# Kernel optimization log

Hardware: AMD Instinct MI355X
Metric: run time of the kernel (lower is better)

Reference implementation:

```python
import jax, jax.numpy as jnp
import numpy as np

HIDDEN = 256
N_HEADS = 8
HEAD_DIM = HIDDEN // N_HEADS
SCALE = HEAD_DIM ** -0.5
LN_EPS = 1e-5


def entmax15(z):
    """Entmax-1.5 along the last axis (Peters et al. 2019 exact algorithm)."""
    z = z / 2.0
    z = z - jnp.max(z, axis=-1, keepdims=True)
    zs = jnp.flip(jnp.sort(z, axis=-1), axis=-1)          # descending
    K = z.shape[-1]
    k = jnp.arange(1, K + 1, dtype=z.dtype)
    mean = jnp.cumsum(zs, axis=-1) / k
    mean_sq = jnp.cumsum(zs * zs, axis=-1) / k
    ss = k * (mean_sq - mean * mean)
    delta = (1.0 - ss) / k
    tau = mean - jnp.sqrt(jnp.maximum(delta, 1e-12))
    support = (tau <= zs).astype(jnp.int32)
    k_star = jnp.sum(support, axis=-1, keepdims=True)      # support size >=1
    tau_star = jnp.take_along_axis(tau, k_star - 1, axis=-1)
    p = jnp.square(jnp.maximum(z - tau_star, 0.0))
    return p


def _attend(q, kv, W_q, W_k, W_v, log_temp):
    B, K, H = kv.shape
    qh = (q @ W_q.T).reshape(B, N_HEADS, HEAD_DIM)                 # (B,n,d)
    kh = (kv @ W_k.T).reshape(B, K, N_HEADS, HEAD_DIM)             # (B,K,n,d)
    vh = (kv @ W_v.T).reshape(B, K, N_HEADS, HEAD_DIM)
    scores = jnp.einsum('bnd,bknd->bnk', qh, kh) * (SCALE * jnp.exp(log_temp))
    attn = entmax15(scores)                                        # (B,n,K) sparse
    ctx = jnp.einsum('bnk,bknd->bnd', attn, vh).reshape(B, H)
    return ctx


def layernorm(x, gamma, beta):
    mu = jnp.mean(x, axis=-1, keepdims=True)
    var = jnp.mean(jnp.square(x - mu), axis=-1, keepdims=True)
    return (x - mu) * jax.lax.rsqrt(var + LN_EPS) * gamma + beta


def setup_inputs() -> dict:
    key = jax.random.key(0)
    ks = jax.random.split(key, 12)
    B, K, H = 32, 8192, HIDDEN
    s = 0.02
    return {
        'z_gene': jax.random.normal(ks[0], (B, H), jnp.float32),
        'z_cpg_seq': jax.random.normal(ks[1], (B, K, H), jnp.float32),
        'z_mirna_seq': jax.random.normal(ks[2], (B, K, H), jnp.float32),
        'W_q': jax.random.normal(ks[3], (H, H), jnp.float32) * s,
        'W_k_cpg': jax.random.normal(ks[4], (H, H), jnp.float32) * s,
        'W_v_cpg': jax.random.normal(ks[5], (H, H), jnp.float32) * s,
        'W_k_mirna': jax.random.normal(ks[6], (H, H), jnp.float32) * s,
        'W_v_mirna': jax.random.normal(ks[7], (H, H), jnp.float32) * s,
        'W_out': jax.random.normal(ks[8], (H, 2 * H), jnp.float32) * s,
        'b_out': jnp.zeros((H,), jnp.float32),
        'ln_gamma': jnp.ones((H,), jnp.float32),
        'ln_beta': jnp.zeros((H,), jnp.float32),
        'modality_logits': jnp.zeros((2,), jnp.float32),
        'log_temp': jnp.zeros((), jnp.float32),
    }


def reference(z_gene, z_cpg_seq, z_mirna_seq, W_q, W_k_cpg, W_v_cpg,
              W_k_mirna, W_v_mirna, W_out, b_out, ln_gamma, ln_beta,
              modality_logits, log_temp):
    ctx_cpg = _attend(z_gene, z_cpg_seq, W_q, W_k_cpg, W_v_cpg, log_temp)
    ctx_mirna = _attend(z_gene, z_mirna_seq, W_q, W_k_mirna, W_v_mirna, log_temp)
    w = jax.nn.softmax(modality_logits)
    combined = jnp.concatenate([w[0] * ctx_cpg, w[1] * ctx_mirna], axis=-1)
    fused = layernorm(combined @ W_out.T + b_out + z_gene, ln_gamma, ln_beta)
    return fused
```

## Files before the change

### kernel.cpp

```cpp
#include <hip/hip_runtime.h>
#include <cstdint>
#include <cstddef>

#define HIDDEN 256
#define NHEADS 8
#define HDIM 32
#define KLEN 8192
#define BATCH 32
#define NCHUNK 16
#define CHUNK (KLEN / NCHUNK)
#define NCHUNK_S 32
#define CROWS (KLEN / NCHUNK_S)
#define LN_EPS 1e-5f

#define OFF_QT   ((size_t)0)
#define SZ_QT    ((size_t)2*BATCH*NHEADS*HIDDEN)
#define OFF_SC   (OFF_QT + SZ_QT)
#define SZ_SC    ((size_t)2*BATCH*KLEN*NHEADS)
#define OFF_UP   (OFF_SC + SZ_SC)
#define SZ_UP    ((size_t)2*BATCH*NCHUNK*NHEADS*HIDDEN)
#define OFF_COMB (OFF_UP + SZ_UP)
#define SZ_COMB  ((size_t)BATCH*2*HIDDEN)

__global__ void k_prep(const float* __restrict__ zg, const float* __restrict__ Wq,
                       const float* __restrict__ Wk0, const float* __restrict__ Wk1,
                       const float* __restrict__ log_temp, float* __restrict__ qt) {
    int b = blockIdx.x, t = threadIdx.x;
    __shared__ float z[HIDDEN];
    __shared__ float qh[HIDDEN];
    z[t] = zg[(size_t)b*HIDDEN + t];
    __syncthreads();
    const float4* wr4 = (const float4*)(Wq + (size_t)t*HIDDEN);
    const float4* z4 = (const float4*)z;
    float acc = 0.f;
    #pragma unroll 8
    for (int i = 0; i < HIDDEN/4; ++i) {
        float4 w = wr4[i], zz = z4[i];
        acc += w.x*zz.x + w.y*zz.y + w.z*zz.z + w.w*zz.w;
    }
    qh[t] = acc;
    __syncthreads();
    float alpha = 0.5f * rsqrtf((float)HDIM) * __expf(log_temp[0]);
    for (int m = 0; m < 2; ++m) {
        const float* Wk = m ? Wk1 : Wk0;
        for (int n = 0; n < NHEADS; ++n) {
            float a = 0.f;
            #pragma unroll 8
            for (int d = 0; d < HDIM; ++d) {
                a += qh[n*HDIM + d] * Wk[(size_t)(n*HDIM + d)*HIDDEN + t];
            }
            qt[(((size_t)m*BATCH + b)*NHEADS + n)*HIDDEN + t] = a * alpha;
        }
    }
}

__global__ void __launch_bounds__(256, 4) k_scores(const float* __restrict__ kv0,
                                                   const float* __restrict__ kv1,
                                                   const float* __restrict__ qt,
                                                   float* __restrict__ sc) {
    int bid = blockIdx.x;
    int chunk = bid % NCHUNK_S;
    int m = (bid / NCHUNK_S) & 1;
    int b = bid / (2*NCHUNK_S);
    int t = threadIdx.x;
    int wave = t >> 6;
    int g    = (t >> 3) & 7;
    int seg  = t & 7;
    __shared__ float lq[NHEADS*260];
    const float* qtg = qt + ((size_t)m*BATCH + b)*NHEADS*HIDDEN;
    #pragma unroll
    for (int i = 0; i < 8; ++i) {
        int j = t + i*256;
        lq[(j >> 8)*260 + (j & 255)] = qtg[j];
    }
    __syncthreads();
    const float* kv = (m ? kv1 : kv0) + (size_t)b*KLEN*HIDDEN;
    const float4* kv4 = (const float4*)kv;
    float* out = sc + ((size_t)m*BATCH + b)*KLEN*NHEADS;
    int b0 = seg & 1, b1 = (seg >> 1) & 1, b2 = (seg >> 2) & 1;

    #pragma unroll
    for (int pass = 0; pass < 2; ++pass) {
        size_t r = (size_t)chunk*CROWS + wave*64 + pass*32 + g*4;
        float acc[4][8];
        #pragma unroll
        for (int j = 0; j < 4; ++j)
            #pragma unroll
            for (int n = 0; n < 8; ++n) acc[j][n] = 0.f;
        #pragma unroll 2
        for (int i = 0; i < 8; ++i) {
            int c = i*8 + seg;
            float4 k0 = kv4[(r+0)*64 + c];
            float4 k1 = kv4[(r+1)*64 + c];
            float4 k2 = kv4[(r+2)*64 + c];
            float4 k3 = kv4[(r+3)*64 + c];
            #pragma unroll
            for (int n = 0; n < 8; ++n) {
                float4 q = ((const float4*)(lq + n*260))[c];
                acc[0][n] += k0.x*q.x + k0.y*q.y + k0.z*q.z + k0.w*q.w;
                acc[1][n] += k1.x*q.x + k1.y*q.y + k1.z*q.z + k1.w*q.w;
                acc[2][n] += k2.x*q.x + k2.y*q.y + k2.z*q.z + k2.w*q.w;
                acc[3][n] += k3.x*q.x + k3.y*q.y + k3.z*q.z + k3.w*q.w;
            }
        }
        #pragma unroll
        for (int j = 0; j < 4; ++j) {
            float w[4];
            #pragma unroll
            for (int u = 0; u < 4; ++u) {
                float kkeep = b0 ? acc[j][2*u+1] : acc[j][2*u];
                float ksend = b0 ? acc[j][2*u]   : acc[j][2*u+1];
                w[u] = kkeep + __shfl_xor(ksend, 1);
            }
            float x[2];
            #pragma unroll
            for (int u = 0; u < 2; ++u) {
                float kkeep = b1 ? w[2*u+1] : w[2*u];
                float ksend = b1 ? w[2*u]   : w[2*u+1];
                x[u] = kkeep + __shfl_xor(ksend, 2);
            }
            float kkeep = b2 ? x[1] : x[0];
            float ksend = b2 ? x[0] : x[1];
            float y = kkeep + __shfl_xor(ksend, 4);
            out[(r+j)*8 + seg] = y;
        }
    }
}

__global__ void __launch_bounds__(256) k_entmax(float* __restrict__ sc) {
    int bid = blockIdx.x;
    int n = bid & 7, b = (bid >> 3) & 31, m = bid >> 8;
    int t = threadIdx.x;
    __shared__ float zs[KLEN];
    __shared__ float red[4];
    float* src = sc + ((size_t)m*BATCH + b)*KLEN*NHEADS + n;
    float mx = -1e30f;
    #pragma unroll
    for (int i = 0; i < KLEN/256; ++i) {
        float v = src[(size_t)(t + i*256)*NHEADS];
        zs[t + i*256] = v;
        mx = fmaxf(mx, v);
    }
    for (int off = 32; off; off >>= 1) mx = fmaxf(mx, __shfl_xor(mx, off));
    if ((t & 63) == 0) red[t >> 6] = mx;
    __syncthreads();
    mx = fmaxf(fmaxf(red[0], red[1]), fmaxf(red[2], red[3]));
    __syncthreads();
    const float4* z4 = (const float4*)zs;
    float lo = mx - 1.0f, hi = mx;
    for (int it = 0; it < 26; ++it) {
        float tm = 0.5f*(lo + hi);
        float s = 0.f;
        #pragma unroll
        for (int i = 0; i < 8; ++i) {
            float4 zz = z4[t + i*256];
            float d;
            d = fmaxf(zz.x - tm, 0.f); s = fmaf(d, d, s);
            d = fmaxf(zz.y - tm, 0.f); s = fmaf(d, d, s);
            d = fmaxf(zz.z - tm, 0.f); s = fmaf(d, d, s);
            d = fmaxf(zz.w - tm, 0.f); s = fmaf(d, d, s);
        }
        for (int off = 32; off; off >>= 1) s += __shfl_xor(s, off);
        if ((t & 63) == 0) red[t >> 6] = s;
        __syncthreads();
        s = red[0] + red[1] + red[2] + red[3];
        __syncthreads();
        if (s >= 1.0f) lo = tm; else hi = tm;
    }
    float tfin = 0.5f*(lo + hi);
    #pragma unroll
    for (int i = 0; i < KLEN/256; ++i) {
        float d = fmaxf(zs[t + i*256] - tfin, 0.f);
        src[(size_t)(t + i*256)*NHEADS] = d*d;
    }
}

__global__ void __launch_bounds__(256, 4) k_ctxsum(const float* __restrict__ kv0,
                                                   const float* __restrict__ kv1,
                                                   const float* __restrict__ sc,
                                                   float* __restrict__ upart) {
    int bid = (int)gridDim.x - 1 - (int)blockIdx.x;
    int chunk = bid % NCHUNK;
    int m = (bid / NCHUNK) & 1;
    int b = bid / (2*NCHUNK);
    int t = threadIdx.x;
    int wave = t >> 6, lane = t & 63;
    const float* kv = (m ? kv1 : kv0) + (size_t)b*KLEN*HIDDEN;
    const float4* kv4 = (const float4*)kv;
    const float4* prow4 = (const float4*)(sc + ((size_t)m*BATCH + b)*KLEN*NHEADS);
    float acc[8][4];
    #pragma unroll
    for (int nn = 0; nn < 8; ++nn)
        #pragma unroll
        for (int c = 0; c < 4; ++c) acc[nn][c] = 0.f;

    for (int kb = wave*4; kb < CHUNK; kb += 16) {
        size_t k = (size_t)chunk*CHUNK + kb;
        float4 kva = kv4[(k+0)*64 + lane];
        float4 kvb = kv4[(k+1)*64 + lane];
        float4 kvc = kv4[(k+2)*64 + lane];
        float4 kvd = kv4[(k+3)*64 + lane];
        float4 pa0 = prow4[(k+0)*2], pa1 = prow4[(k+0)*2 + 1];
        float4 pb0 = prow4[(k+1)*2], pb1 = prow4[(k+1)*2 + 1];
        float4 pc0 = prow4[(k+2)*2], pc1 = prow4[(k+2)*2 + 1];
        float4 pd0 = prow4[(k+3)*2], pd1 = prow4[(k+3)*2 + 1];
        #define ACC4(P0, P1, KV) \
            acc[0][0] = fmaf(P0.x, KV.x, acc[0][0]); acc[0][1] = fmaf(P0.x, KV.y, acc[0][1]); \
            acc[0][2] = fmaf(P0.x, KV.z, acc[0][2]); acc[0][3] = fmaf(P0.x, KV.w, acc[0][3]); \
            acc[1][0] = fmaf(P0.y, KV.x, acc[1][0]); acc[1][1] = fmaf(P0.y, KV.y, acc[1][1]); \
            acc[1][2] = fmaf(P0.y, KV.z, acc[1][2]); acc[1][3] = fmaf(P0.y, KV.w, acc[1][3]); \
            acc[2][0] = fmaf(P0.z, KV.x, acc[2][0]); acc[2][1] = fmaf(P0.z, KV.y, acc[2][1]); \
            acc[2][2] = fmaf(P0.z, KV.z, acc[2][2]); acc[2][3] = fmaf(P0.z, KV.w, acc[2][3]); \
            acc[3][0] = fmaf(P0.w, KV.x, acc[3][0]); acc[3][1] = fmaf(P0.w, KV.y, acc[3][1]); \
            acc[3][2] = fmaf(P0.w, KV.z, acc[3][2]); acc[3][3] = fmaf(P0.w, KV.w, acc[3][3]); \
            acc[4][0] = fmaf(P1.x, KV.x, acc[4][0]); acc[4][1] = fmaf(P1.x, KV.y, acc[4][1]); \
            acc[4][2] = fmaf(P1.x, KV.z, acc[4][2]); acc[4][3] = fmaf(P1.x, KV.w, acc[4][3]); \
            acc[5][0] = fmaf(P1.y, KV.x, acc[5][0]); acc[5][1] = fmaf(P1.y, KV.y, acc[5][1]); \
            acc[5][2] = fmaf(P1.y, KV.z, acc[5][2]); acc[5][3] = fmaf(P1.y, KV.w, acc[5][3]); \
            acc[6][0] = fmaf(P1.z, KV.x, acc[6][0]); acc[6][1] = fmaf(P1.z, KV.y, acc[6][1]); \
            acc[6][2] = fmaf(P1.z, KV.z, acc[6][2]); acc[6][3] = fmaf(P1.z, KV.w, acc[6][3]); \
            acc[7][0] = fmaf(P1.w, KV.x, acc[7][0]); acc[7][1] = fmaf(P1.w, KV.y, acc[7][1]); \
            acc[7][2] = fmaf(P1.w, KV.z, acc[7][2]); acc[7][3] = fmaf(P1.w, KV.w, acc[7][3]);
        ACC4(pa0, pa1, kva)
        ACC4(pb0, pb1, kvb)
        ACC4(pc0, pc1, kvc)
        ACC4(pd0, pd1, kvd)
        #undef ACC4
    }
    __shared__ float redls[4*NHEADS*HIDDEN];
    float4* red4 = (float4*)redls;
    #pragma unroll
    for (int nn = 0; nn < 8; ++nn) {
        float4 v; v.x = acc[nn][0]; v.y = acc[nn][1]; v.z = acc[nn][2]; v.w = acc[nn][3];
        red4[((size_t)wave*8 + nn)*64 + lane] = v;
    }
    __syncthreads();
    float* up = upart + (((size_t)m*BATCH + b)*NCHUNK + chunk)*NHEADS*HIDDEN;
    int n = t >> 5, hq = (t & 31)*2;
    #pragma unroll
    for (int j = 0; j < 2; ++j) {
        float4 s = red4[((size_t)0*8 + n)*64 + hq + j];
        #pragma unroll
        for (int w = 1; w < 4; ++w) {
            float4 v = red4[((size_t)w*8 + n)*64 + hq + j];
            s.x += v.x; s.y += v.y; s.z += v.z; s.w += v.w;
        }
        ((float4*)(up + (size_t)n*HIDDEN))[hq + j] = s;
    }
}

__global__ void k_ctx(const float* __restrict__ upart, const float* __restrict__ Wv0,
                      const float* __restrict__ Wv1, const float* __restrict__ mlogits,
                      float* __restrict__ comb) {
    int b = blockIdx.x, t = threadIdx.x;
    __shared__ float ul[NHEADS*260];
    float l0 = mlogits[0], l1 = mlogits[1];
    float mxl = fmaxf(l0, l1);
    float e0 = __expf(l0 - mxl), e1 = __expf(l1 - mxl);
    float w0 = e0/(e0 + e1), w1 = e1/(e0 + e1);
    for (int m = 0; m < 2; ++m) {
        const float* Wv = m ? Wv1 : Wv0;
        float wm = m ? w1 : w0;
        __syncthreads();
        for (int n = 0; n < NHEADS; ++n) {
            float s = 0.f;
            const float* up = upart + ((size_t)m*BATCH + b)*NCHUNK*NHEADS*HIDDEN
                              + (size_t)n*HIDDEN + t;
            #pragma unroll
            for (int c = 0; c < NCHUNK; ++c) s += up[(size_t)c*NHEADS*HIDDEN];
            ul[n*260 + t] = s;
        }
        __syncthreads();
        int n = t >> 5;
        const float4* wr4 = (const float4*)(Wv + (size_t)t*HIDDEN);
        const float4* uu4 = (const float4*)(ul + n*260);
        float acc = 0.f;
        #pragma unroll 8
        for (int i = 0; i < HIDDEN/4; ++i) {
            float4 w = wr4[i], uu = uu4[i];
            acc += w.x*uu.x + w.y*uu.y + w.z*uu.z + w.w*uu.w;
        }
        comb[(size_t)b*(2*HIDDEN) + (size_t)m*HIDDEN + t] = acc * wm;
    }
}

__global__ void k_out(const float* __restrict__ comb, const float* __restrict__ Wout,
                      const float* __restrict__ bout, const float* __restrict__ zg,
                      const float* __restrict__ gamma, const float* __restrict__ beta,
                      float* __restrict__ out) {
    int b = blockIdx.x, t = threadIdx.x;
    __shared__ float cl[2*HIDDEN];
    __shared__ float red[4];
    cl[t] = comb[(size_t)b*512 + t];
    cl[t + 256] = comb[(size_t)b*512 + 256 + t];
    __syncthreads();
    float acc = bout[t] + zg[(size_t)b*HIDDEN + t];
    const float4* wr4 = (const float4*)(Wout + (size_t)t*512);
    const float4* cl4 = (const float4*)cl;
    #pragma unroll 8
    for (int i = 0; i < 512/4; ++i) {
        float4 w = wr4[i], c = cl4[i];
        acc += w.x*c.x + w.y*c.y + w.z*c.z + w.w*c.w;
    }
    float s = acc;
    for (int off = 32; off; off >>= 1) s += __shfl_xor(s, off);
    if ((t & 63) == 0) red[t >> 6] = s;
    __syncthreads();
    float mu = (red[0] + red[1] + red[2] + red[3]) * (1.0f/HIDDEN);
    __syncthreads();
    float dv = acc - mu;
    float vs = dv*dv;
    for (int off = 32; off; off >>= 1) vs += __shfl_xor(vs, off);
    if ((t & 63) == 0) red[t >> 6] = vs;
    __syncthreads();
    float var = (red[0] + red[1] + red[2] + red[3]) * (1.0f/HIDDEN);
    out[(size_t)b*HIDDEN + t] = dv * rsqrtf(var + LN_EPS) * gamma[t] + beta[t];
}

extern "C" void kernel_launch(void* const* d_in, const int* in_sizes, int n_in,
                              void* d_out, int out_size, void* d_ws, size_t ws_size,
                              hipStream_t stream) {
    const float* zg    = (const float*)d_in[0];
    const float* cpg   = (const float*)d_in[1];
    const float* mir   = (const float*)d_in[2];
    const float* Wq    = (const float*)d_in[3];
    const float* Wk0   = (const float*)d_in[4];
    const float* Wv0   = (const float*)d_in[5];
    const float* Wk1   = (const float*)d_in[6];
    const float* Wv1   = (const float*)d_in[7];
    const float* Wout  = (const float*)d_in[8];
    const float* bout  = (const float*)d_in[9];
    const float* gam   = (const float*)d_in[10];
    const float* bet   = (const float*)d_in[11];
    const float* mlog  = (const float*)d_in[12];
    const float* ltemp = (const float*)d_in[13];

    float* ws   = (float*)d_ws;
    float* qt   = ws + OFF_QT;
    float* sc   = ws + OFF_SC;
    float* up   = ws + OFF_UP;
    float* comb = ws + OFF_COMB;
    float* out  = (float*)d_out;

    hipLaunchKernelGGL(k_prep,   dim3(BATCH),             dim3(256), 0, stream,
                       zg, Wq, Wk0, Wk1, ltemp, qt);
    hipLaunchKernelGGL(k_scores, dim3(BATCH*2*NCHUNK_S),  dim3(256), 0, stream,
                       cpg, mir, qt, sc);
    hipLaunchKernelGGL(k_entmax, dim3(2*BATCH*NHEADS),    dim3(256), 0, stream,
                       sc);
    hipLaunchKernelGGL(k_ctxsum, dim3(BATCH*2*NCHUNK),    dim3(256), 0, stream,
                       cpg, mir, sc, up);
    hipLaunchKernelGGL(k_ctx,    dim3(BATCH),             dim3(256), 0, stream,
                       up, Wv0, Wv1, mlog, comb);
    hipLaunchKernelGGL(k_out,    dim3(BATCH),             dim3(256), 0, stream,
                       comb, Wout, bout, zg, gam, bet, out);
}
```

Baseline: 338.4 us.

## Compact entmax support rows and gather only nonzero rows in context sum

Adds a k_support kernel that builds, per (modality, batch), a compacted list of key rows where any head has nonzero entmax weight. k_ctxsum then reads only those rows instead of streaming the full 8192-row KV. The aim is to cut the second full read of the KV tensors, since entmax output is sparse. k_scores is also restructured: more chunks, a single pass per thread, and manual software pipelining of the loads. The cost is an extra launch, a serial scan in k_support, and scattered row reads whose speed depends on how sparse the weights are.

```diff
diff --git a/kernel.cpp b/kernel.cpp
--- a/kernel.cpp
+++ b/kernel.cpp
@@ -7,20 +7,23 @@
 #define HDIM 32
 #define KLEN 8192
 #define BATCH 32
-#define NCHUNK 16
-#define CHUNK (KLEN / NCHUNK)
-#define NCHUNK_S 32
+#define NCHUNK_S 64
 #define CROWS (KLEN / NCHUNK_S)
+#define NSPLIT 8
 #define LN_EPS 1e-5f
 
-#define OFF_QT   ((size_t)0)
-#define SZ_QT    ((size_t)2*BATCH*NHEADS*HIDDEN)
-#define OFF_SC   (OFF_QT + SZ_QT)
-#define SZ_SC    ((size_t)2*BATCH*KLEN*NHEADS)
-#define OFF_UP   (OFF_SC + SZ_SC)
-#define SZ_UP    ((size_t)2*BATCH*NCHUNK*NHEADS*HIDDEN)
-#define OFF_COMB (OFF_UP + SZ_UP)
-#define SZ_COMB  ((size_t)BATCH*2*HIDDEN)
+#define OFF_QT    ((size_t)0)
+#define SZ_QT     ((size_t)2*BATCH*NHEADS*HIDDEN)
+#define OFF_SC    (OFF_QT + SZ_QT)
+#define SZ_SC     ((size_t)2*BATCH*KLEN*NHEADS)
+#define OFF_UP    (OFF_SC + SZ_SC)
+#define SZ_UP     ((size_t)2*BATCH*NSPLIT*NHEADS*HIDDEN)
+#define OFF_COMB  (OFF_UP + SZ_UP)
+#define SZ_COMB   ((size_t)BATCH*2*HIDDEN)
+#define OFF_SLIST (OFF_COMB + SZ_COMB)
+#define SZ_SLIST  ((size_t)2*BATCH*KLEN)
+#define OFF_SCNT  (OFF_SLIST + SZ_SLIST)
+#define SZ_SCNT   ((size_t)2*BATCH)
 
 __global__ void k_prep(const float* __restrict__ zg, const float* __restrict__ Wq,
                        const float* __restrict__ Wk0, const float* __restrict__ Wk1,
@@ -63,9 +66,8 @@
     int m = (bid / NCHUNK_S) & 1;
     int b = bid / (2*NCHUNK_S);
     int t = threadIdx.x;
-    int wave = t >> 6;
-    int g    = (t >> 3) & 7;
-    int seg  = t & 7;
+    int gg  = t >> 3;
+    int seg = t & 7;
     __shared__ float lq[NHEADS*260];
     const float* qtg = qt + ((size_t)m*BATCH + b)*NHEADS*HIDDEN;
     #pragma unroll
@@ -79,51 +81,65 @@
     float* out = sc + ((size_t)m*BATCH + b)*KLEN*NHEADS;
     int b0 = seg & 1, b1 = (seg >> 1) & 1, b2 = (seg >> 2) & 1;
 
-    #pragma unroll
-    for (int pass = 0; pass < 2; ++pass) {
-        size_t r = (size_t)chunk*CROWS + wave*64 + pass*32 + g*4;
-        float acc[4][8];
-        #pragma unroll
-        for (int j = 0; j < 4; ++j)
-            #pragma unroll
-            for (int n = 0; n < 8; ++n) acc[j][n] = 0.f;
-        #pragma unroll 2
-        for (int i = 0; i < 8; ++i) {
-            int c = i*8 + seg;
-            float4 k0 = kv4[(r+0)*64 + c];
-            float4 k1 = kv4[(r+1)*64 + c];
-            float4 k2 = kv4[(r+2)*64 + c];
-            float4 k3 = kv4[(r+3)*64 + c];
-            #pragma unroll
-            for (int n = 0; n < 8; ++n) {
-                float4 q = ((const float4*)(lq + n*260))[c];
-                acc[0][n] += k0.x*q.x + k0.y*q.y + k0.z*q.z + k0.w*q.w;
-                acc[1][n] += k1.x*q.x + k1.y*q.y + k1.z*q.z + k1.w*q.w;
-                acc[2][n] += k2.x*q.x + k2.y*q.y + k2.z*q.z + k2.w*q.w;
-                acc[3][n] += k3.x*q.x + k3.y*q.y + k3.z*q.z + k3.w*q.w;
-            }
-        }
-        #pragma unroll
-        for (int j = 0; j < 4; ++j) {
-            float w[4];
-            #pragma unroll
-            for (int u = 0; u < 4; ++u) {
-                float kkeep = b0 ? acc[j][2*u+1] : acc[j][2*u];
-                float ksend = b0 ? acc[j][2*u]   : acc[j][2*u+1];
-                w[u] = kkeep + __shfl_xor(ksend, 1);
-            }
-            float x[2];
-            #pragma unroll
-            for (int u = 0; u < 2; ++u) {
-                float kkeep = b1 ? w[2*u+1] : w[2*u];
-                float ksend = b1 ? w[2*u]   : w[2*u+1];
-                x[u] = kkeep + __shfl_xor(ksend, 2);
-            }
-            float kkeep = b2 ? x[1] : x[0];
-            float ksend = b2 ? x[0] : x[1];
-            float y = kkeep + __shfl_xor(ksend, 4);
-            out[(r+j)*8 + seg] = y;
-        }
+    size_t r = (size_t)chunk*CROWS + gg*4;
+    const float4* row0 = kv4 + (r+0)*64;
+    const float4* row1 = kv4 + (r+1)*64;
+    const float4* row2 = kv4 + (r+2)*64;
+    const float4* row3 = kv4 + (r+3)*64;
+
+    float acc[4][8];
+    #pragma unroll
+    for (int j = 0; j < 4; ++j)
+        #pragma unroll
+        for (int n = 0; n < 8; ++n) acc[j][n] = 0.f;
+
+    float4 A0,A1,A2,A3, B0,B1,B2,B3, C0,C1,C2,C3, D0,D1,D2,D3;
+    #define LOADQ(R0,R1,R2,R3,i) { int c = (i)*8 + seg; \
+        R0 = row0[c]; R1 = row1[c]; R2 = row2[c]; R3 = row3[c]; }
+    #define FMAQ(R0,R1,R2,R3,i) { int c = (i)*8 + seg; \
+        _Pragma("unroll") \
+        for (int n = 0; n < 8; ++n) { \
+            float4 q = ((const float4*)(lq + n*260))[c]; \
+            acc[0][n] += R0.x*q.x + R0.y*q.y + R0.z*q.z + R0.w*q.w; \
+            acc[1][n] += R1.x*q.x + R1.y*q.y + R1.z*q.z + R1.w*q.w; \
+            acc[2][n] += R2.x*q.x + R2.y*q.y + R2.z*q.z + R2.w*q.w; \
+            acc[3][n] += R3.x*q.x + R3.y*q.y + R3.z*q.z + R3.w*q.w; } }
+
+    LOADQ(A0,A1,A2,A3,0)
+    LOADQ(B0,B1,B2,B3,1)
+    LOADQ(C0,C1,C2,C3,2)
+    LOADQ(D0,D1,D2,D3,3)
+    FMAQ(A0,A1,A2,A3,0) LOADQ(A0,A1,A2,A3,4)
+    FMAQ(B0,B1,B2,B3,1) LOADQ(B0,B1,B2,B3,5)
+    FMAQ(C0,C1,C2,C3,2) LOADQ(C0,C1,C2,C3,6)
+    FMAQ(D0,D1,D2,D3,3) LOADQ(D0,D1,D2,D3,7)
+    FMAQ(A0,A1,A2,A3,4)
+    FMAQ(B0,B1,B2,B3,5)
+    FMAQ(C0,C1,C2,C3,6)
+    FMAQ(D0,D1,D2,D3,7)
+    #undef LOADQ
+    #undef FMAQ
+
+    #pragma unroll
+    for (int j = 0; j < 4; ++j) {
+        float w[4];
+        #pragma unroll
+        for (int u = 0; u < 4; ++u) {
+            float kkeep = b0 ? acc[j][2*u+1] : acc[j][2*u];
+            float ksend = b0 ? acc[j][2*u]   : acc[j][2*u+1];
+            w[u] = kkeep + __shfl_xor(ksend, 1);
+        }
+        float x[2];
+        #pragma unroll
+        for (int u = 0; u < 2; ++u) {
+            float kkeep = b1 ? w[2*u+1] : w[2*u];
+            float ksend = b1 ? w[2*u]   : w[2*u+1];
+            x[u] = kkeep + __shfl_xor(ksend, 2);
+        }
+        float kkeep = b2 ? x[1] : x[0];
+        float ksend = b2 ? x[0] : x[1];
+        float y = kkeep + __shfl_xor(ksend, 4);
+        out[(r+j)*8 + seg] = y;
     }
 }
 
@@ -175,57 +191,79 @@
     }
 }
 
-__global__ void __launch_bounds__(256, 4) k_ctxsum(const float* __restrict__ kv0,
-                                                   const float* __restrict__ kv1,
-                                                   const float* __restrict__ sc,
-                                                   float* __restrict__ upart) {
-    int bid = (int)gridDim.x - 1 - (int)blockIdx.x;
-    int chunk = bid % NCHUNK;
-    int m = (bid / NCHUNK) & 1;
-    int b = bid / (2*NCHUNK);
+__global__ void __launch_bounds__(256) k_support(const float* __restrict__ sc,
+                                                 int* __restrict__ slist,
+                                                 int* __restrict__ scnt) {
+    int mb = blockIdx.x;
+    int t = threadIdx.x;
+    int lane = t & 63, w = t >> 6;
+    __shared__ int wcnt[4];
+    const float4* p4 = (const float4*)(sc + (size_t)mb*KLEN*NHEADS);
+    int* list = slist + (size_t)mb*KLEN;
+    int base = 0;
+    for (int i = 0; i < KLEN/256; ++i) {
+        int k = i*256 + t;
+        float4 pa = p4[(size_t)k*2];
+        float4 pb = p4[(size_t)k*2 + 1];
+        float mxp = fmaxf(fmaxf(fmaxf(pa.x, pa.y), fmaxf(pa.z, pa.w)),
+                          fmaxf(fmaxf(pb.x, pb.y), fmaxf(pb.z, pb.w)));
+        bool f = (mxp > 0.f);
+        unsigned long long mask = __ballot(f);
+        if (lane == 0) wcnt[w] = __popcll(mask);
+        __syncthreads();
+        int wbase = base;
+        #pragma unroll
+        for (int wi = 0; wi < 4; ++wi) if (wi < w) wbase += wcnt[wi];
+        if (f) list[wbase + __popcll(mask & ((1ull << lane) - 1ull))] = k;
+        base += wcnt[0] + wcnt[1] + wcnt[2] + wcnt[3];
+        __syncthreads();
+    }
+    if (t == 0) scnt[mb] = base;
+}
+
+__global__ void __launch_bounds__(256) k_ctxsum(const float* __restrict__ kv0,
+                                                const float* __restrict__ kv1,
+                                                const float* __restrict__ sc,
+                                                const int* __restrict__ slist,
+                                                const int* __restrict__ scnt,
+                                                float* __restrict__ upart) {
+    int bid = blockIdx.x;
+    int s = bid % NSPLIT;
+    int mb = bid / NSPLIT;
     int t = threadIdx.x;
     int wave = t >> 6, lane = t & 63;
-    const float* kv = (m ? kv1 : kv0) + (size_t)b*KLEN*HIDDEN;
+    const float* kv = ((mb >> 5) ? kv1 : kv0) + (size_t)(mb & 31)*KLEN*HIDDEN;
     const float4* kv4 = (const float4*)kv;
-    const float4* prow4 = (const float4*)(sc + ((size_t)m*BATCH + b)*KLEN*NHEADS);
+    const float4* p4 = (const float4*)(sc + (size_t)mb*KLEN*NHEADS);
+    const int* list = slist + (size_t)mb*KLEN;
+    int cnt = scnt[mb];
     float acc[8][4];
     #pragma unroll
     for (int nn = 0; nn < 8; ++nn)
         #pragma unroll
         for (int c = 0; c < 4; ++c) acc[nn][c] = 0.f;
 
-    for (int kb = wave*4; kb < CHUNK; kb += 16) {
-        size_t k = (size_t)chunk*CHUNK + kb;
-        float4 kva = kv4[(k+0)*64 + lane];
-        float4 kvb = kv4[(k+1)*64 + lane];
-        float4 kvc = kv4[(k+2)*64 + lane];
-        float4 kvd = kv4[(k+3)*64 + lane];
-        float4 pa0 = prow4[(k+0)*2], pa1 = prow4[(k+0)*2 + 1];
-        float4 pb0 = prow4[(k+1)*2], pb1 = prow4[(k+1)*2 + 1];
-        float4 pc0 = prow4[(k+2)*2], pc1 = prow4[(k+2)*2 + 1];
-        float4 pd0 = prow4[(k+3)*2], pd1 = prow4[(k+3)*2 + 1];
-        #define ACC4(P0, P1, KV) \
-            acc[0][0] = fmaf(P0.x, KV.x, acc[0][0]); acc[0][1] = fmaf(P0.x, KV.y, acc[0][1]); \
-            acc[0][2] = fmaf(P0.x, KV.z, acc[0][2]); acc[0][3] = fmaf(P0.x, KV.w, acc[0][3]); \
-            acc[1][0] = fmaf(P0.y, KV.x, acc[1][0]); acc[1][1] = fmaf(P0.y, KV.y, acc[1][1]); \
-            acc[1][2] = fmaf(P0.y, KV.z, acc[1][2]); acc[1][3] = fmaf(P0.y, KV.w, acc[1][3]); \
-            acc[2][0] = fmaf(P0.z, KV.x, acc[2][0]); acc[2][1] = fmaf(P0.z, KV.y, acc[2][1]); \
-            acc[2][2] = fmaf(P0.z, KV.z, acc[2][2]); acc[2][3] = fmaf(P0.z, KV.w, acc[2][3]); \
-            acc[3][0] = fmaf(P0.w, KV.x, acc[3][0]); acc[3][1] = fmaf(P0.w, KV.y, acc[3][1]); \
-            acc[3][2] = fmaf(P0.w, KV.z, acc[3][2]); acc[3][3] = fmaf(P0.w, KV.w, acc[3][3]); \
-            acc[4][0] = fmaf(P1.x, KV.x, acc[4][0]); acc[4][1] = fmaf(P1.x, KV.y, acc[4][1]); \
-            acc[4][2] = fmaf(P1.x, KV.z, acc[4][2]); acc[4][3] = fmaf(P1.x, KV.w, acc[4][3]); \
-            acc[5][0] = fmaf(P1.y, KV.x, acc[5][0]); acc[5][1] = fmaf(P1.y, KV.y, acc[5][1]); \
-            acc[5][2] = fmaf(P1.y, KV.z, acc[5][2]); acc[5][3] = fmaf(P1.y, KV.w, acc[5][3]); \
-            acc[6][0] = fmaf(P1.z, KV.x, acc[6][0]); acc[6][1] = fmaf(P1.z, KV.y, acc[6][1]); \
-            acc[6][2] = fmaf(P1.z, KV.z, acc[6][2]); acc[6][3] = fmaf(P1.z, KV.w, acc[6][3]); \
-            acc[7][0] = fmaf(P1.w, KV.x, acc[7][0]); acc[7][1] = fmaf(P1.w, KV.y, acc[7][1]); \
-            acc[7][2] = fmaf(P1.w, KV.z, acc[7][2]); acc[7][3] = fmaf(P1.w, KV.w, acc[7][3]);
-        ACC4(pa0, pa1, kva)
-        ACC4(pb0, pb1, kvb)
-        ACC4(pc0, pc1, kvc)
-        ACC4(pd0, pd1, kvd)
-        #undef ACC4
+    for (int j = s + NSPLIT*wave; j < cnt; j += NSPLIT*4) {
+        int k = list[j];
+        float4 kvv = kv4[(size_t)k*64 + lane];
+        float4 p0 = p4[(size_t)k*2];
+        float4 p1 = p4[(size_t)k*2 + 1];
+        acc[0][0] = fmaf(p0.x, kvv.x, acc[0][0]); acc[0][1] = fmaf(p0.x, kvv.y, acc[0][1]);
+        acc[0][2] = fmaf(p0.x, kvv.z, acc[0][2]); acc[0][3] = fmaf(p0.x, kvv.w, acc[0][3]);
+        acc[1][0] = fmaf(p0.y, kvv.x, acc[1][0]); acc[1][1] = fmaf(p0.y, kvv.y, acc[1][1]);
+        acc[1][2] = fmaf(p0.y, kvv.z, acc[1][2]); acc[1][3] = fmaf(p0.y, kvv.w, acc[1][3]);
+        acc[2][0] = fmaf(p0.z, kvv.x, acc[2][0]); acc[2][1] = fmaf(p0.z, kvv.y, acc[2][1]);
+        acc[2][2] = fmaf(p0.z, kvv.z, acc[2][2]); acc[2][3] = fmaf(p0.z, kvv.w, acc[2][3]);
+        acc[3][0] = fmaf(p0.w, kvv.x, acc[3][0]); acc[3][1] = fmaf(p0.w, kvv.y, acc[3][1]);
+        acc[3][2] = fmaf(p0.w, kvv.z, acc[3][2]); acc[3][3] = fmaf(p0.w, kvv.w, acc[3][3]);
+        acc[4][0] = fmaf(p1.x, kvv.x, acc[4][0]); acc[4][1] = fmaf(p1.x, kvv.y, acc[4][1]);
+        acc[4][2] = fmaf(p1.x, kvv.z, acc[4][2]); acc[4][3] = fmaf(p1.x, kvv.w, acc[4][3]);
+        acc[5][0] = fmaf(p1.y, kvv.x, acc[5][0]); acc[5][1] = fmaf(p1.y, kvv.y, acc[5][1]);
+        acc[5][2] = fmaf(p1.y, kvv.z, acc[5][2]); acc[5][3] = fmaf(p1.y, kvv.w, acc[5][3]);
+        acc[6][0] = fmaf(p1.z, kvv.x, acc[6][0]); acc[6][1] = fmaf(p1.z, kvv.y, acc[6][1]);
+        acc[6][2] = fmaf(p1.z, kvv.z, acc[6][2]); acc[6][3] = fmaf(p1.z, kvv.w, acc[6][3]);
+        acc[7][0] = fmaf(p1.w, kvv.x, acc[7][0]); acc[7][1] = fmaf(p1.w, kvv.y, acc[7][1]);
+        acc[7][2] = fmaf(p1.w, kvv.z, acc[7][2]); acc[7][3] = fmaf(p1.w, kvv.w, acc[7][3]);
     }
     __shared__ float redls[4*NHEADS*HIDDEN];
     float4* red4 = (float4*)redls;
@@ -235,17 +273,17 @@
         red4[((size_t)wave*8 + nn)*64 + lane] = v;
     }
     __syncthreads();
-    float* up = upart + (((size_t)m*BATCH + b)*NCHUNK + chunk)*NHEADS*HIDDEN;
+    float* up = upart + ((size_t)mb*NSPLIT + s)*NHEADS*HIDDEN;
     int n = t >> 5, hq = (t & 31)*2;
     #pragma unroll
     for (int j = 0; j < 2; ++j) {
-        float4 s = red4[((size_t)0*8 + n)*64 + hq + j];
+        float4 sum = red4[((size_t)0*8 + n)*64 + hq + j];
         #pragma unroll
         for (int w = 1; w < 4; ++w) {
             float4 v = red4[((size_t)w*8 + n)*64 + hq + j];
-            s.x += v.x; s.y += v.y; s.z += v.z; s.w += v.w;
-        }
-        ((float4*)(up + (size_t)n*HIDDEN))[hq + j] = s;
+            sum.x += v.x; sum.y += v.y; sum.z += v.z; sum.w += v.w;
+        }
+        ((float4*)(up + (size_t)n*HIDDEN))[hq + j] = sum;
     }
 }
 
@@ -264,10 +302,10 @@
         __syncthreads();
         for (int n = 0; n < NHEADS; ++n) {
             float s = 0.f;
-            const float* up = upart + ((size_t)m*BATCH + b)*NCHUNK*NHEADS*HIDDEN
+            const float* up = upart + ((size_t)m*BATCH + b)*NSPLIT*NHEADS*HIDDEN
                               + (size_t)n*HIDDEN + t;
             #pragma unroll
-            for (int c = 0; c < NCHUNK; ++c) s += up[(size_t)c*NHEADS*HIDDEN];
+            for (int c = 0; c < NSPLIT; ++c) s += up[(size_t)c*NHEADS*HIDDEN];
             ul[n*260 + t] = s;
         }
         __syncthreads();
@@ -335,23 +373,27 @@
     const float* mlog  = (const float*)d_in[12];
     const float* ltemp = (const float*)d_in[13];
 
-    float* ws   = (float*)d_ws;
-    float* qt   = ws + OFF_QT;
-    float* sc   = ws + OFF_SC;
-    float* up   = ws + OFF_UP;
-    float* comb = ws + OFF_COMB;
-    float* out  = (float*)d_out;
-
-    hipLaunchKernelGGL(k_prep,   dim3(BATCH),             dim3(256), 0, stream,
+    float* ws    = (float*)d_ws;
+    float* qt    = ws + OFF_QT;
+    float* sc    = ws + OFF_SC;
+    float* up    = ws + OFF_UP;
+    float* comb  = ws + OFF_COMB;
+    int*   slist = (int*)(ws + OFF_SLIST);
+    int*   scnt  = (int*)(ws + OFF_SCNT);
+    float* out   = (float*)d_out;
+
+    hipLaunchKernelGGL(k_prep,    dim3(BATCH),             dim3(256), 0, stream,
                        zg, Wq, Wk0, Wk1, ltemp, qt);
-    hipLaunchKernelGGL(k_scores, dim3(BATCH*2*NCHUNK_S),  dim3(256), 0, stream,
+    hipLaunchKernelGGL(k_scores,  dim3(BATCH*2*NCHUNK_S),  dim3(256), 0, stream,
                        cpg, mir, qt, sc);
-    hipLaunchKernelGGL(k_entmax, dim3(2*BATCH*NHEADS),    dim3(256), 0, stream,
+    hipLaunchKernelGGL(k_entmax,  dim3(2*BATCH*NHEADS),    dim3(256), 0, stream,
                        sc);
-    hipLaunchKernelGGL(k_ctxsum, dim3(BATCH*2*NCHUNK),    dim3(256), 0, stream,
-                       cpg, mir, sc, up);
-    hipLaunchKernelGGL(k_ctx,    dim3(BATCH),             dim3(256), 0, stream,
+    hipLaunchKernelGGL(k_support, dim3(2*BATCH),           dim3(256), 0, stream,
+                       sc, slist, scnt);
+    hipLaunchKernelGGL(k_ctxsum,  dim3(2*BATCH*NSPLIT),    dim3(256), 0, stream,
+                       cpg, mir, sc, slist, scnt, up);
+    hipLaunchKernelGGL(k_ctx,     dim3(BATCH),             dim3(256), 0, stream,
                        up, Wv0, Wv1, mlog, comb);
-    hipLaunchKernelGGL(k_out,    dim3(BATCH),             dim3(256), 0, stream,
+    hipLaunchKernelGGL(k_out,     dim3(BATCH),             dim3(256), 0, stream,
                        comb, Wout, bout, zg, gam, bet, out);
 }
```

Result: slower. 419.5 us (+24.0%).

## Rewrite score kernel to one-row-per-wave with register q and prefetch; simplify ctxsum loop

Applied to the files above, without the earlier changes.

The score kernel now keeps the q vectors in registers instead of shared memory. Each wave processes one key row per iteration, with a full-row load coalesced across 64 lanes and a software prefetch of the next row, and the result is reduced by a butterfly shuffle across the whole wave. The ctxsum kernel drops the 4-row unrolled body for a single row per wave iteration, removes the occupancy launch bound and the reversed block order. This aims for more coalesced loads and less LDS traffic, at the cost of more shuffles per row and less ILP per thread.

```diff
diff --git a/kernel.cpp b/kernel.cpp
--- a/kernel.cpp
+++ b/kernel.cpp
@@ -9,18 +9,17 @@
 #define BATCH 32
 #define NCHUNK 16
 #define CHUNK (KLEN / NCHUNK)
-#define NCHUNK_S 32
-#define CROWS (KLEN / NCHUNK_S)
+#define NSLAB 32
 #define LN_EPS 1e-5f
 
-#define OFF_QT   ((size_t)0)
-#define SZ_QT    ((size_t)2*BATCH*NHEADS*HIDDEN)
-#define OFF_SC   (OFF_QT + SZ_QT)
-#define SZ_SC    ((size_t)2*BATCH*KLEN*NHEADS)
-#define OFF_UP   (OFF_SC + SZ_SC)
-#define SZ_UP    ((size_t)2*BATCH*NCHUNK*NHEADS*HIDDEN)
-#define OFF_COMB (OFF_UP + SZ_UP)
-#define SZ_COMB  ((size_t)BATCH*2*HIDDEN)
+#define OFF_QT    ((size_t)0)
+#define SZ_QT     ((size_t)2*BATCH*NHEADS*HIDDEN)
+#define OFF_SC    (OFF_QT + SZ_QT)
+#define SZ_SC     ((size_t)2*BATCH*KLEN*NHEADS)
+#define OFF_UP    (OFF_SC + SZ_SC)
+#define SZ_UP     ((size_t)2*BATCH*NCHUNK*NHEADS*HIDDEN)
+#define OFF_COMB  (OFF_UP + SZ_UP)
+#define SZ_COMB   ((size_t)BATCH*2*HIDDEN)
 
 __global__ void k_prep(const float* __restrict__ zg, const float* __restrict__ Wq,
                        const float* __restrict__ Wk0, const float* __restrict__ Wk1,
@@ -59,71 +58,52 @@
                                                    const float* __restrict__ qt,
                                                    float* __restrict__ sc) {
     int bid = blockIdx.x;
-    int chunk = bid % NCHUNK_S;
-    int m = (bid / NCHUNK_S) & 1;
-    int b = bid / (2*NCHUNK_S);
+    int slab = bid & (NSLAB - 1);
+    int mb = bid / NSLAB;
     int t = threadIdx.x;
-    int wave = t >> 6;
-    int g    = (t >> 3) & 7;
-    int seg  = t & 7;
-    __shared__ float lq[NHEADS*260];
-    const float* qtg = qt + ((size_t)m*BATCH + b)*NHEADS*HIDDEN;
-    #pragma unroll
-    for (int i = 0; i < 8; ++i) {
-        int j = t + i*256;
-        lq[(j >> 8)*260 + (j & 255)] = qtg[j];
-    }
-    __syncthreads();
-    const float* kv = (m ? kv1 : kv0) + (size_t)b*KLEN*HIDDEN;
+    int wave = t >> 6, l = t & 63;
+    const float* kv = ((mb >> 5) ? kv1 : kv0) + (size_t)(mb & 31)*KLEN*HIDDEN;
     const float4* kv4 = (const float4*)kv;
-    float* out = sc + ((size_t)m*BATCH + b)*KLEN*NHEADS;
-    int b0 = seg & 1, b1 = (seg >> 1) & 1, b2 = (seg >> 2) & 1;
-
-    #pragma unroll
-    for (int pass = 0; pass < 2; ++pass) {
-        size_t r = (size_t)chunk*CROWS + wave*64 + pass*32 + g*4;
-        float acc[4][8];
-        #pragma unroll
-        for (int j = 0; j < 4; ++j)
-            #pragma unroll
-            for (int n = 0; n < 8; ++n) acc[j][n] = 0.f;
-        #pragma unroll 2
-        for (int i = 0; i < 8; ++i) {
-            int c = i*8 + seg;
-            float4 k0 = kv4[(r+0)*64 + c];
-            float4 k1 = kv4[(r+1)*64 + c];
-            float4 k2 = kv4[(r+2)*64 + c];
-            float4 k3 = kv4[(r+3)*64 + c];
-            #pragma unroll
-            for (int n = 0; n < 8; ++n) {
-                float4 q = ((const float4*)(lq + n*260))[c];
-                acc[0][n] += k0.x*q.x + k0.y*q.y + k0.z*q.z + k0.w*q.w;
-                acc[1][n] += k1.x*q.x + k1.y*q.y + k1.z*q.z + k1.w*q.w;
-                acc[2][n] += k2.x*q.x + k2.y*q.y + k2.z*q.z + k2.w*q.w;
-                acc[3][n] += k3.x*q.x + k3.y*q.y + k3.z*q.z + k3.w*q.w;
-            }
-        }
-        #pragma unroll
-        for (int j = 0; j < 4; ++j) {
-            float w[4];
-            #pragma unroll
-            for (int u = 0; u < 4; ++u) {
-                float kkeep = b0 ? acc[j][2*u+1] : acc[j][2*u];
-                float ksend = b0 ? acc[j][2*u]   : acc[j][2*u+1];
-                w[u] = kkeep + __shfl_xor(ksend, 1);
-            }
-            float x[2];
-            #pragma unroll
-            for (int u = 0; u < 2; ++u) {
-                float kkeep = b1 ? w[2*u+1] : w[2*u];
-                float ksend = b1 ? w[2*u]   : w[2*u+1];
-                x[u] = kkeep + __shfl_xor(ksend, 2);
-            }
-            float kkeep = b2 ? x[1] : x[0];
-            float ksend = b2 ? x[0] : x[1];
-            float y = kkeep + __shfl_xor(ksend, 4);
-            out[(r+j)*8 + seg] = y;
-        }
+    const float* qtg = qt + (size_t)mb*NHEADS*HIDDEN;
+    float4 qreg[8];
+    #pragma unroll
+    for (int n = 0; n < 8; ++n)
+        qreg[n] = *(const float4*)(qtg + (size_t)n*HIDDEN + 4*l);
+    float* out = sc + (size_t)mb*KLEN*NHEADS;
+    int b0 = l & 1, b1 = (l >> 1) & 1, b2 = (l >> 2) & 1;
+
+    int k = slab*256 + wave;
+    float4 cur = kv4[(size_t)k*64 + l];
+    #pragma unroll 2
+    for (int i = 0; i < 64; ++i) {
+        float4 nxt = cur;
+        if (i < 63) nxt = kv4[(size_t)(k + 4)*64 + l];
+        float a[8];
+        #pragma unroll
+        for (int n = 0; n < 8; ++n)
+            a[n] = cur.x*qreg[n].x + cur.y*qreg[n].y + cur.z*qreg[n].z + cur.w*qreg[n].w;
+        float w[4];
+        #pragma unroll
+        for (int u = 0; u < 4; ++u) {
+            float keep = b0 ? a[2*u+1] : a[2*u];
+            float send = b0 ? a[2*u]   : a[2*u+1];
+            w[u] = keep + __shfl_xor(send, 1);
+        }
+        float x[2];
+        #pragma unroll
+        for (int u = 0; u < 2; ++u) {
+            float keep = b1 ? w[2*u+1] : w[2*u];
+            float send = b1 ? w[2*u]   : w[2*u+1];
+            x[u] = keep + __shfl_xor(send, 2);
+        }
+        float keep = b2 ? x[1] : x[0];
+        float send = b2 ? x[0] : x[1];
+        float y = keep + __shfl_xor(send, 4);
+        y += __shfl_xor(y, 8);
+        y += __shfl_xor(y, 16);
+        y += __shfl_xor(y, 32);
+        if (l < 8) out[(size_t)k*8 + l] = y;
+        cur = nxt; k += 4;
     }
 }
 
@@ -175,11 +155,11 @@
     }
 }
 
-__global__ void __launch_bounds__(256, 4) k_ctxsum(const float* __restrict__ kv0,
-                                                   const float* __restrict__ kv1,
-                                                   const float* __restrict__ sc,
-                                                   float* __restrict__ upart) {
-    int bid = (int)gridDim.x - 1 - (int)blockIdx.x;
+__global__ void __launch_bounds__(256) k_ctxsum(const float* __restrict__ kv0,
+                                                const float* __restrict__ kv1,
+                                                const float* __restrict__ sc,
+                                                float* __restrict__ upart) {
+    int bid = blockIdx.x;
     int chunk = bid % NCHUNK;
     int m = (bid / NCHUNK) & 1;
     int b = bid / (2*NCHUNK);
@@ -190,49 +170,38 @@
     const float4* prow4 = (const float4*)(sc + ((size_t)m*BATCH + b)*KLEN*NHEADS);
     float acc[8][4];
     #pragma unroll
-    for (int nn = 0; nn < 8; ++nn)
-        #pragma unroll
-        for (int c = 0; c < 4; ++c) acc[nn][c] = 0.f;
-
-    for (int kb = wave*4; kb < CHUNK; kb += 16) {
-        size_t k = (size_t)chunk*CHUNK + kb;
-        float4 kva = kv4[(k+0)*64 + lane];
-        float4 kvb = kv4[(k+1)*64 + lane];
-        float4 kvc = kv4[(k+2)*64 + lane];
-        float4 kvd = kv4[(k+3)*64 + lane];
-        float4 pa0 = prow4[(k+0)*2], pa1 = prow4[(k+0)*2 + 1];
-        float4 pb0 = prow4[(k+1)*2], pb1 = prow4[(k+1)*2 + 1];
-        float4 pc0 = prow4[(k+2)*2], pc1 = prow4[(k+2)*2 + 1];
-        float4 pd0 = prow4[(k+3)*2], pd1 = prow4[(k+3)*2 + 1];
-        #define ACC4(P0, P1, KV) \
-            acc[0][0] = fmaf(P0.x, KV.x, acc[0][0]); acc[0][1] = fmaf(P0.x, KV.y, acc[0][1]); \
-            acc[0][2] = fmaf(P0.x, KV.z, acc[0][2]); acc[0][3] = fmaf(P0.x, KV.w, acc[0][3]); \
-            acc[1][0] = fmaf(P0.y, KV.x, acc[1][0]); acc[1][1] = fmaf(P0.y, KV.y, acc[1][1]); \
-            acc[1][2] = fmaf(P0.y, KV.z, acc[1][2]); acc[1][3] = fmaf(P0.y, KV.w, acc[1][3]); \
-            acc[2][0] = fmaf(P0.z, KV.x, acc[2][0]); acc[2][1] = fmaf(P0.z, KV.y, acc[2][1]); \
-            acc[2][2] = fmaf(P0.z, KV.z, acc[2][2]); acc[2][3] = fmaf(P0.z, KV.w, acc[2][3]); \
-            acc[3][0] = fmaf(P0.w, KV.x, acc[3][0]); acc[3][1] = fmaf(P0.w, KV.y, acc[3][1]); \
-            acc[3][2] = fmaf(P0.w, KV.z, acc[3][2]); acc[3][3] = fmaf(P0.w, KV.w, acc[3][3]); \
-            acc[4][0] = fmaf(P1.x, KV.x, acc[4][0]); acc[4][1] = fmaf(P1.x, KV.y, acc[4][1]); \
-            acc[4][2] = fmaf(P1.x, KV.z, acc[4][2]); acc[4][3] = fmaf(P1.x, KV.w, acc[4][3]); \
-            acc[5][0] = fmaf(P1.y, KV.x, acc[5][0]); acc[5][1] = fmaf(P1.y, KV.y, acc[5][1]); \
-            acc[5][2] = fmaf(P1.y, KV.z, acc[5][2]); acc[5][3] = fmaf(P1.y, KV.w, acc[5][3]); \
-            acc[6][0] = fmaf(P1.z, KV.x, acc[6][0]); acc[6][1] = fmaf(P1.z, KV.y, acc[6][1]); \
-            acc[6][2] = fmaf(P1.z, KV.z, acc[6][2]); acc[6][3] = fmaf(P1.z, KV.w, acc[6][3]); \
-            acc[7][0] = fmaf(P1.w, KV.x, acc[7][0]); acc[7][1] = fmaf(P1.w, KV.y, acc[7][1]); \
-            acc[7][2] = fmaf(P1.w, KV.z, acc[7][2]); acc[7][3] = fmaf(P1.w, KV.w, acc[7][3]);
-        ACC4(pa0, pa1, kva)
-        ACC4(pb0, pb1, kvb)
-        ACC4(pc0, pc1, kvc)
-        ACC4(pd0, pd1, kvd)
-        #undef ACC4
+    for (int n = 0; n < 8; ++n)
+        #pragma unroll
+        for (int c = 0; c < 4; ++c) acc[n][c] = 0.f;
+
+    #pragma unroll 2
+    for (int kk = wave; kk < CHUNK; kk += 4) {
+        size_t k = (size_t)chunk*CHUNK + kk;
+        float4 kvv = kv4[k*64 + lane];
+        float4 p0 = prow4[k*2], p1 = prow4[k*2 + 1];
+        acc[0][0] = fmaf(p0.x, kvv.x, acc[0][0]); acc[0][1] = fmaf(p0.x, kvv.y, acc[0][1]);
+        acc[0][2] = fmaf(p0.x, kvv.z, acc[0][2]); acc[0][3] = fmaf(p0.x, kvv.w, acc[0][3]);
+        acc[1][0] = fmaf(p0.y, kvv.x, acc[1][0]); acc[1][1] = fmaf(p0.y, kvv.y, acc[1][1]);
+        acc[1][2] = fmaf(p0.y, kvv.z, acc[1][2]); acc[1][3] = fmaf(p0.y, kvv.w, acc[1][3]);
+        acc[2][0] = fmaf(p0.z, kvv.x, acc[2][0]); acc[2][1] = fmaf(p0.z, kvv.y, acc[2][1]);
+        acc[2][2] = fmaf(p0.z, kvv.z, acc[2][2]); acc[2][3] = fmaf(p0.z, kvv.w, acc[2][3]);
+        acc[3][0] = fmaf(p0.w, kvv.x, acc[3][0]); acc[3][1] = fmaf(p0.w, kvv.y, acc[3][1]);
+        acc[3][2] = fmaf(p0.w, kvv.z, acc[3][2]); acc[3][3] = fmaf(p0.w, kvv.w, acc[3][3]);
+        acc[4][0] = fmaf(p1.x, kvv.x, acc[4][0]); acc[4][1] = fmaf(p1.x, kvv.y, acc[4][1]);
+        acc[4][2] = fmaf(p1.x, kvv.z, acc[4][2]); acc[4][3] = fmaf(p1.x, kvv.w, acc[4][3]);
+        acc[5][0] = fmaf(p1.y, kvv.x, acc[5][0]); acc[5][1] = fmaf(p1.y, kvv.y, acc[5][1]);
+        acc[5][2] = fmaf(p1.y, kvv.z, acc[5][2]); acc[5][3] = fmaf(p1.y, kvv.w, acc[5][3]);
+        acc[6][0] = fmaf(p1.z, kvv.x, acc[6][0]); acc[6][1] = fmaf(p1.z, kvv.y, acc[6][1]);
+        acc[6][2] = fmaf(p1.z, kvv.z, acc[6][2]); acc[6][3] = fmaf(p1.z, kvv.w, acc[6][3]);
+        acc[7][0] = fmaf(p1.w, kvv.x, acc[7][0]); acc[7][1] = fmaf(p1.w, kvv.y, acc[7][1]);
+        acc[7][2] = fmaf(p1.w, kvv.z, acc[7][2]); acc[7][3] = fmaf(p1.w, kvv.w, acc[7][3]);
     }
     __shared__ float redls[4*NHEADS*HIDDEN];
     float4* red4 = (float4*)redls;
     #pragma unroll
-    for (int nn = 0; nn < 8; ++nn) {
-        float4 v; v.x = acc[nn][0]; v.y = acc[nn][1]; v.z = acc[nn][2]; v.w = acc[nn][3];
-        red4[((size_t)wave*8 + nn)*64 + lane] = v;
+    for (int n = 0; n < 8; ++n) {
+        float4 v; v.x = acc[n][0]; v.y = acc[n][1]; v.z = acc[n][2]; v.w = acc[n][3];
+        red4[((size_t)wave*8 + n)*64 + lane] = v;
     }
     __syncthreads();
     float* up = upart + (((size_t)m*BATCH + b)*NCHUNK + chunk)*NHEADS*HIDDEN;
@@ -342,16 +311,16 @@
     float* comb = ws + OFF_COMB;
     float* out  = (float*)d_out;
 
-    hipLaunchKernelGGL(k_prep,   dim3(BATCH),             dim3(256), 0, stream,
+    hipLaunchKernelGGL(k_prep,   dim3(BATCH),           dim3(256), 0, stream,
                        zg, Wq, Wk0, Wk1, ltemp, qt);
-    hipLaunchKernelGGL(k_scores, dim3(BATCH*2*NCHUNK_S),  dim3(256), 0, stream,
+    hipLaunchKernelGGL(k_scores, dim3(2*BATCH*NSLAB),   dim3(256), 0, stream,
                        cpg, mir, qt, sc);
-    hipLaunchKernelGGL(k_entmax, dim3(2*BATCH*NHEADS),    dim3(256), 0, stream,
+    hipLaunchKernelGGL(k_entmax, dim3(2*BATCH*NHEADS),  dim3(256), 0, stream,
                        sc);
-    hipLaunchKernelGGL(k_ctxsum, dim3(BATCH*2*NCHUNK),    dim3(256), 0, stream,
+    hipLaunchKernelGGL(k_ctxsum, dim3(BATCH*2*NCHUNK),  dim3(256), 0, stream,
                        cpg, mir, sc, up);
-    hipLaunchKernelGGL(k_ctx,    dim3(BATCH),             dim3(256), 0, stream,
+    hipLaunchKernelGGL(k_ctx,    dim3(BATCH),           dim3(256), 0, stream,
                        up, Wv0, Wv1, mlog, comb);
-    hipLaunchKernelGGL(k_out,    dim3(BATCH),             dim3(256), 0, stream,
+    hipLaunchKernelGGL(k_out,    dim3(BATCH),           dim3(256), 0, stream,
                        comb, Wout, bout, zg, gam, bet, out);
 }
```

Result: slower. 368.6 us (+8.9%).
